# Kernel tuning notes

Measured on AMD Instinct MI355X. Metric: run time of the kernel, lower is better.

The kernel has to match this reference:

```python
import jax, jax.numpy as jnp
import numpy as np

CURVE = 1.0
TAU = 0.5
NB_RF = 64


def _mnorm(x):
    # Minkowski (Lorentz) inner product of x with itself, keepdims: [..., 1]
    return -x[..., :1] ** 2 + jnp.sum(x[..., 1:] ** 2, axis=-1, keepdims=True)


def _hyp_linear(x, W, b, c=CURVE):
    # HypLinear: linear map on space part, time recomputed to stay on hyperboloid.
    # x: [N, Din], W: [H, Din, Ds], b: [H, Ds] -> [H, N, Ds+1]
    space = jnp.einsum('nd,hds->hns', x, W) + b[:, None, :]
    time = jnp.sqrt(1.0 / c + jnp.sum(space ** 2, axis=-1, keepdims=True))
    return jnp.concatenate([time, space], axis=-1)


def _softmax_kernel(data, proj, tau=TAU, c=CURVE, eps=1e-8):
    # FAVOR+ style positive random-feature transform with hyperbolic time correction.
    t = data[..., :1]          # [H, N, 1] Lorentz time component
    s = data[..., 1:]          # [H, N, D-1] space components
    m = 1.0 / jnp.sqrt(jnp.float32(proj.shape[0]))
    wx = jnp.exp(jnp.einsum('hnd,dm->hnm', s, proj) / jnp.sqrt(jnp.float32(tau)))
    front = jnp.exp(((1.0 / c) / tau - t ** 2 / tau) / 2.0) * m + eps
    return wx * front          # [H, N, NB_RF]


def _kernelized(q, k, v, proj, c=CURVE):
    # O(N) linear attention: sum_n k'(n) v(n) then q' @ summary, plus Lorentz renorm.
    qp = _softmax_kernel(q, proj)
    kp = _softmax_kernel(k, proj)
    last = jnp.einsum('hnm,hnd->hmd', kp, v)      # [H, NB_RF, D]
    z = jnp.einsum('hnm,hmd->hnd', qp, last)      # [H, Nq, D]
    coeff = (1.0 / jnp.sqrt(c)) / jnp.sqrt(jnp.abs(_mnorm(z) + 1e-7))
    return z * coeff


def _mobius_add(a, b, c=CURVE):
    ab = jnp.sum(a * b, axis=-1, keepdims=True)
    a2 = jnp.sum(a * a, axis=-1, keepdims=True)
    b2 = jnp.sum(b * b, axis=-1, keepdims=True)
    num = (1.0 + 2.0 * c * ab + c * b2) * a + (1.0 - c * a2) * b
    den = 1.0 + 2.0 * c * ab + c * c * a2 * b2
    return num / (den + 1e-7)


def _hyper_agg(t, c=CURVE):
    # hyperbolic_mean with uniform 1/H weights: Lorentz centroid over heads.
    m = jnp.mean(t, axis=0)                       # [N, D]
    return jnp.sqrt(1.0 / c) * m / jnp.sqrt(jnp.abs(_mnorm(m)) + 1e-7)


def setup_inputs() -> dict:
    H, Din, Ds = 4, 257, 256
    Nu, Ni = 20000, 20000
    # Structured projection matrix: vstacked transposed orthogonal 64x64 blocks,
    # rows rescaled by chi-distributed norms (scaling=0 in the torch code).
    rng = np.random.default_rng(0)
    blocks = []
    for _ in range(Ds // NB_RF):
        q, _ = np.linalg.qr(rng.standard_normal((NB_RF, NB_RF)))
        blocks.append(q.T)
    final = np.vstack(blocks)                     # [Ds, NB_RF]
    mult = np.linalg.norm(rng.standard_normal((Ds, NB_RF)), axis=1)
    proj = jnp.asarray((mult[:, None] * final).astype(np.float32))
    key = jax.random.key(0)
    ks = jax.random.split(key, 5)
    u = jax.random.normal(ks[0], (Nu, Din), dtype=jnp.float32) * 0.3
    i = jax.random.normal(ks[1], (Ni, Din), dtype=jnp.float32) * 0.3
    Wk = jax.random.normal(ks[2], (H, Din, Ds), dtype=jnp.float32) * 0.01
    Wq = jax.random.normal(ks[3], (H, Din, Ds), dtype=jnp.float32) * 0.01
    Wv = jax.random.normal(ks[4], (H, Din, Ds), dtype=jnp.float32) * 0.01
    bk = jnp.zeros((H, Ds), dtype=jnp.float32)
    bq = jnp.zeros((H, Ds), dtype=jnp.float32)
    bv = jnp.zeros((H, Ds), dtype=jnp.float32)
    return {"u": u, "i": i, "Wk": Wk, "bk": bk, "Wq": Wq, "bq": bq,
            "Wv": Wv, "bv": bv, "proj": proj}


def reference(u, i, Wk, bk, Wq, bq, Wv, bv, proj):
    u_key = _hyp_linear(u, Wk, bk)
    i_key = _hyp_linear(i, Wk, bk)
    u_query = _hyp_linear(u, Wq, bq)
    i_query = _hyp_linear(i, Wq, bq)
    u_value = _hyp_linear(u, Wv, bv)
    i_value = _hyp_linear(i, Wv, bv)
    _u_value = _kernelized(u_query, i_key, i_value, proj)
    _i_value = _kernelized(i_query, u_key, u_value, proj)
    u_out = _mobius_add(u_value, _u_value)
    i_out = _mobius_add(i_value, _i_value)
    return _hyper_agg(u_out), _hyper_agg(i_out)
```

## Files before the change

kernel.cpp:

```cpp
#include <hip/hip_runtime.h>
#include <hip/hip_bf16.h>

#define HH 4
#define NR 20000
#define DIN 257
#define DS 256
#define MF 64
#define KP 288
#define VP 264
#define LTP 272
#define ZST 276
#define LKC 25

typedef __bf16 bf16;
typedef bf16 bf16x8 __attribute__((ext_vector_type(8)));
typedef bf16 bf16x4 __attribute__((ext_vector_type(4)));
typedef bf16 bf16x2 __attribute__((ext_vector_type(2)));
typedef float f32x4 __attribute__((ext_vector_type(4)));
typedef unsigned int u32x4 __attribute__((ext_vector_type(4)));

__global__ void cvt_x_kernel(const float* __restrict__ xA, const float* __restrict__ xB,
                             bf16* __restrict__ xbA, bf16* __restrict__ xbB) {
  const int n = blockIdx.x, k = threadIdx.x;
  const float* x = blockIdx.y ? xB : xA;
  bf16* xb = blockIdx.y ? xbB : xbA;
  bf16 v = (bf16)0.f;
  if (k < DIN) v = (bf16)x[(long)n * DIN + k];
  else if (k == DIN) v = (bf16)1.f;
  xb[(long)n * KP + k] = v;
}

__global__ void cvt_w_kernel(const float* __restrict__ Wq, const float* __restrict__ Wk,
                             const float* __restrict__ Wv, bf16* __restrict__ WbTq,
                             bf16* __restrict__ WbTk, bf16* __restrict__ WbTv) {
  const int which = blockIdx.y;
  const int h = blockIdx.x >> 8, n = blockIdx.x & 255, k = threadIdx.x;
  const float* W = which == 0 ? Wq : (which == 1 ? Wk : Wv);
  bf16* o = which == 0 ? WbTq : (which == 1 ? WbTk : WbTv);
  o[((long)h * 256 + n) * KP + k] =
      (k < DIN) ? (bf16)W[((long)h * DIN + k) * DS + n] : (bf16)0.f;
}

__global__ void cvt_wp_kernel(const float* __restrict__ Wq, const float* __restrict__ Wk,
                              const float* __restrict__ bq, const float* __restrict__ bk,
                              const float* __restrict__ proj, bf16* __restrict__ WpT) {
  const int k = blockIdx.x, h = blockIdx.y, which = blockIdx.z, m = threadIdx.x;
  const float* W = which ? Wk : Wq;
  const float* bb = which ? bk : bq;
  float acc = 0.f;
  if (k < DIN) {
    const float* wr = W + ((long)h * DIN + k) * DS;
#pragma unroll 8
    for (int d = 0; d < DS; d++) acc = fmaf(wr[d], proj[(long)d * MF + m], acc);
  } else if (k == DIN) {
    const float* br = bb + (long)h * DS;
#pragma unroll 8
    for (int d = 0; d < DS; d++) acc = fmaf(br[d], proj[(long)d * MF + m], acc);
  }
  WpT[(((long)which * HH + h) * MF + m) * KP + k] = (bf16)acc;
}

__device__ __forceinline__ void gl_lds16(const bf16* g, bf16* l) {
  __builtin_amdgcn_global_load_lds(
      (const __attribute__((address_space(1))) unsigned int*)g,
      (__attribute__((address_space(3))) unsigned int*)l, 16, 0, 0);
}

__global__ __launch_bounds__(256) void proj4_kernel(
    const bf16* __restrict__ xbA, const bf16* __restrict__ xbB,
    const bf16* __restrict__ WbTq, const bf16* __restrict__ WbTk,
    const bf16* __restrict__ WbTv,
    const float* __restrict__ bq, const float* __restrict__ bk,
    const float* __restrict__ bv,
    bf16* __restrict__ voA, bf16* __restrict__ voB, float* __restrict__ fr)
{
  __shared__ __align__(16) char smem[40960];
  bf16* Ab = (bf16*)smem;
  bf16* Bb = (bf16*)(smem + 8192);
  float (*rs)[4] = (float(*)[4])smem;

  const int t = threadIdx.x;
  const int zh = blockIdx.x;
  const int h = zh & 3;
  const int z = zh >> 2;
  const int n0 = blockIdx.y * 64;
  const bf16* xb = (z == 1 || z >= 4) ? xbB : xbA;
  const bf16* WbT = (z < 2) ? WbTv : ((z == 2 || z == 4) ? WbTq : WbTk);
  const float* bsel = (z < 2) ? bv : ((z == 2 || z == 4) ? bq : bk);
  const int w = t >> 6, lane = t & 63;
  const int m16 = lane & 15, q = lane >> 4;
  const bf16* wbh = WbT + (long)h * 256 * KP;

  const int rsub = w * 16 + (lane >> 2);
  const int cb = (lane & 3) * 8;
  const bf16* gA = xb + (long)min(n0 + rsub, NR - 1) * KP + cb;
  const bf16* gB = wbh + (long)rsub * KP + cb;

#define STAGE(buf, c)                                                        \
  do {                                                                       \
    const int _k0 = (c) * 32;                                                \
    gl_lds16(gA + _k0, Ab + (buf) * 2048 + w * 512);                         \
    _Pragma("unroll")                                                        \
    for (int e = 0; e < 4; e++)                                              \
      gl_lds16(gB + (long)e * 64 * KP + _k0,                                 \
               Bb + (buf) * 8192 + e * 2048 + w * 512);                      \
  } while (0)

  f32x4 acc[4][4] = {};
  STAGE(0, 0);

  for (int c = 0; c < 9; c++) {
    const int cur = c & 1;
    __syncthreads();
    if (c < 8) STAGE(1 - cur, c + 1);

    bf16x8 af[4], bfj[4];
#pragma unroll
    for (int i = 0; i < 4; i++)
      af[i] = *(const bf16x8*)(Ab + cur * 2048 + (i * 16 + m16) * 32 + q * 8);
#pragma unroll
    for (int j = 0; j < 4; j++)
      bfj[j] = *(const bf16x8*)(Bb + cur * 8192 + (w * 64 + j * 16 + m16) * 32 + q * 8);
#pragma unroll
    for (int i = 0; i < 4; i++)
#pragma unroll
      for (int j = 0; j < 4; j++)
        acc[i][j] = __builtin_amdgcn_mfma_f32_16x16x32_bf16(af[i], bfj[j], acc[i][j], 0, 0, 0);
  }
#undef STAGE

  __syncthreads();

  float bias[4];
#pragma unroll
  for (int j = 0; j < 4; j++) bias[j] = bsel[h * DS + w * 64 + j * 16 + m16];
#pragma unroll
  for (int i = 0; i < 4; i++)
#pragma unroll
    for (int r = 0; r < 4; r++) {
      float s = 0.f;
#pragma unroll
      for (int j = 0; j < 4; j++) {
        acc[i][j][r] += bias[j];
        s = fmaf(acc[i][j][r], acc[i][j][r], s);
      }
      for (int off = 1; off < 16; off <<= 1) s += __shfl_xor(s, off);
      if (m16 == 0) rs[i * 16 + q * 4 + r][w] = s;
    }
  __syncthreads();

  if (z < 2) {
    bf16* vout = z ? voB : voA;
    if (t < 64) {
      const float ss = rs[t][0] + rs[t][1] + rs[t][2] + rs[t][3];
      if (n0 + t < NR) vout[((long)h * NR + n0 + t) * VP] = (bf16)sqrtf(1.f + ss);
    }
#pragma unroll
    for (int i = 0; i < 4; i++) {
      const int row = i * 16 + q * 4;
#pragma unroll
      for (int r = 0; r < 4; r++) {
        const int rg = n0 + row + r;
        if (rg < NR) {
          bf16* vo = vout + ((long)h * NR + rg) * VP + 1 + w * 64 + m16;
          vo[0] = (bf16)acc[i][0][r]; vo[16] = (bf16)acc[i][1][r];
          vo[32] = (bf16)acc[i][2][r]; vo[48] = (bf16)acc[i][3][r];
        }
      }
    }
  } else {
    if (t < 64 && n0 + t < NR) {
      const float ss = rs[t][0] + rs[t][1] + rs[t][2] + rs[t][3];
      fr[((long)(z - 2) * HH + h) * NR + n0 + t] = 0.125f * __expf(-ss) + 1e-8f;
    }
  }
}

__global__ __launch_bounds__(256) void feat_kernel(
    const bf16* __restrict__ xbA, const bf16* __restrict__ xbB,
    const bf16* __restrict__ WpT, const float* __restrict__ fr,
    bf16* __restrict__ qpA, bf16* __restrict__ kpA,
    bf16* __restrict__ qpB, bf16* __restrict__ kpB)
{
  const int t = threadIdx.x;
  const int ch = blockIdx.x;
  const int h = ch & 3;
  const int c = ch >> 2;
  const int n0 = blockIdx.y * 128;
  const bf16* xb = (c >= 2) ? xbB : xbA;
  const bf16* wp = WpT + (((long)(c & 1) * HH + h) * MF) * KP;
  bf16* fout = (c == 0) ? qpA : (c == 1) ? kpA : (c == 2) ? qpB : kpB;
  const float* frc = fr + ((long)c * HH + h) * NR;
  const int w = t >> 6, lane = t & 63;
  const int m16 = lane & 15, q = lane >> 4;
  const int r0 = w * 32;

  const bf16* aptr[2];
#pragma unroll
  for (int i = 0; i < 2; i++)
    aptr[i] = xb + (long)min(n0 + r0 + i * 16 + m16, NR - 1) * KP + q * 8;
  const bf16* bptr[4];
#pragma unroll
  for (int j = 0; j < 4; j++)
    bptr[j] = wp + (long)(j * 16 + m16) * KP + q * 8;

  f32x4 acc[2][4] = {};
  bf16x8 afc[2], bfc[4], afn[2], bfn[4];
#pragma unroll
  for (int i = 0; i < 2; i++) afc[i] = *(const bf16x8*)(aptr[i]);
#pragma unroll
  for (int j = 0; j < 4; j++) bfc[j] = *(const bf16x8*)(bptr[j]);

  for (int c9 = 0; c9 < 9; c9++) {
    if (c9 < 8) {
      const int k1 = (c9 + 1) * 32;
#pragma unroll
      for (int i = 0; i < 2; i++) afn[i] = *(const bf16x8*)(aptr[i] + k1);
#pragma unroll
      for (int j = 0; j < 4; j++) bfn[j] = *(const bf16x8*)(bptr[j] + k1);
    }
#pragma unroll
    for (int i = 0; i < 2; i++)
#pragma unroll
      for (int j = 0; j < 4; j++)
        acc[i][j] = __builtin_amdgcn_mfma_f32_16x16x32_bf16(afc[i], bfc[j], acc[i][j], 0, 0, 0);
#pragma unroll
    for (int i = 0; i < 2; i++) afc[i] = afn[i];
#pragma unroll
    for (int j = 0; j < 4; j++) bfc[j] = bfn[j];
  }
  const float SQ2 = 1.41421356237309515f;
#pragma unroll
  for (int i = 0; i < 2; i++)
#pragma unroll
    for (int r = 0; r < 4; r++) {
      const int rg = n0 + r0 + i * 16 + q * 4 + r;
      if (rg < NR) {
        const float frv = frc[rg];
        bf16* fo = fout + ((long)h * NR + rg) * MF + m16;
#pragma unroll
        for (int j = 0; j < 4; j++)
          fo[j * 16] = (bf16)(__expf(SQ2 * acc[i][j][r]) * frv);
      }
    }
}

__global__ __launch_bounds__(256) void last3_kernel(
    const bf16* __restrict__ vA, const bf16* __restrict__ fA,
    const bf16* __restrict__ vB, const bf16* __restrict__ fB,
    float* __restrict__ part)
{
  __shared__ unsigned int Va[64 * 17];
  __shared__ unsigned int Fa[64 * 17];
  const int t = threadIdx.x;
  const int dt = blockIdx.x, kc = blockIdx.y, z = blockIdx.z;
  const int side = z >> 2, h = z & 3;
  const bf16* v = side ? vB : vA;
  const bf16* f = side ? fB : fA;
  const int d0 = dt * 64;
  const int w = t >> 6, lane = t & 63;
  const int m16 = lane & 15, q = lane >> 4;
  const int np = t >> 4, xg = (t & 15) * 4;
  f32x4 acc[4] = {};

  for (int c = 0; c < LKC; c++) {
    const int n0 = (kc * LKC + c) * 32;
    {
      const bf16* s0 = v + ((long)h * NR + n0 + 2 * np) * VP + d0 + xg;
      const bf16* s1 = s0 + VP;
      if (d0 + xg + 3 < DIN) {
        const bf16x4 a0 = *(const bf16x4*)s0;
        const bf16x4 a1 = *(const bf16x4*)s1;
#pragma unroll
        for (int e = 0; e < 4; e++) {
          bf16x2 p; p[0] = a0[e]; p[1] = a1[e];
          Va[(xg + e) * 17 + np] = __builtin_bit_cast(unsigned int, p);
        }
      } else {
#pragma unroll
        for (int e = 0; e < 4; e++) {
          bf16 a0 = (bf16)0.f, a1 = (bf16)0.f;
          if (d0 + xg + e < DIN) { a0 = s0[e]; a1 = s1[e]; }
          bf16x2 p; p[0] = a0; p[1] = a1;
          Va[(xg + e) * 17 + np] = __builtin_bit_cast(unsigned int, p);
        }
      }
    }
    {
      const bf16* s0 = f + ((long)h * NR + n0 + 2 * np) * MF + xg;
      const bf16x4 f0 = *(const bf16x4*)s0;
      const bf16x4 f1 = *(const bf16x4*)(s0 + MF);
#pragma unroll
      for (int e = 0; e < 4; e++) {
        bf16x2 p; p[0] = f0[e]; p[1] = f1[e];
        Fa[(xg + e) * 17 + np] = __builtin_bit_cast(unsigned int, p);
      }
    }
    __syncthreads();
    u32x4 bw;
#pragma unroll
    for (int c4 = 0; c4 < 4; c4++) bw[c4] = Fa[(w * 16 + m16) * 17 + q * 4 + c4];
    const bf16x8 bv = __builtin_bit_cast(bf16x8, bw);
#pragma unroll
    for (int i = 0; i < 4; i++) {
      u32x4 aw;
#pragma unroll
      for (int c4 = 0; c4 < 4; c4++) aw[c4] = Va[(i * 16 + m16) * 17 + q * 4 + c4];
      acc[i] = __builtin_amdgcn_mfma_f32_16x16x32_bf16(
          __builtin_bit_cast(bf16x8, aw), bv, acc[i], 0, 0, 0);
    }
    __syncthreads();
  }
  float* pp = part + ((long)(z * LKC + kc) * 5 + dt) * 4096;
#pragma unroll
  for (int i = 0; i < 4; i++)
#pragma unroll
    for (int r = 0; r < 4; r++)
      pp[(i * 16 + q * 4 + r) * 64 + w * 16 + m16] = acc[i][r];
}

__global__ void reduce_last4(const float* __restrict__ part,
                             bf16* __restrict__ hiU, bf16* __restrict__ loU,
                             bf16* __restrict__ hiI, bf16* __restrict__ loI) {
  const int d = blockIdx.x, zz = blockIdx.y, m = threadIdx.x;
  const int side = zz >> 2, h = zz & 3;
  const int dt = d >> 6, dl = d & 63;
  float s = 0.f;
#pragma unroll 5
  for (int kc = 0; kc < LKC; kc++)
    s += part[((long)(zz * LKC + kc) * 5 + dt) * 4096 + dl * 64 + m];
  bf16* hi = side ? hiI : hiU;
  bf16* lo = side ? loI : loU;
  const bf16 hv = (bf16)s;
  hi[((long)h * LTP + d) * MF + m] = hv;
  lo[((long)h * LTP + d) * MF + m] = (bf16)(s - (float)hv);
}

__global__ __launch_bounds__(256) void fuse3_kernel(
    const bf16* __restrict__ qpA, const bf16* __restrict__ vA,
    const bf16* __restrict__ hiA, const bf16* __restrict__ loA,
    const bf16* __restrict__ qpB, const bf16* __restrict__ vB,
    const bf16* __restrict__ hiB, const bf16* __restrict__ loB,
    float* __restrict__ out)
{
  __shared__ __align__(16) float zs[32 * ZST];

  const int side = blockIdx.y;
  const bf16* qp = side ? qpB : qpA;
  const bf16* v = side ? vB : vA;
  const bf16* hi = side ? hiB : hiA;
  const bf16* lo = side ? loB : loA;
  float* o = out + (long)side * NR * DIN;

  const int t = threadIdx.x;
  const int n0 = blockIdx.x * 32;
  const int w = t >> 6, lane = t & 63;
  const int m16 = lane & 15, q = lane >> 4;
  const int erow = t >> 3, ecol = (t & 7) * 4;
  const bool lead = ((t & 7) == 0);
  const int ntile = (w == 0) ? 5 : 4;

  f32x4 macc[8] = {};
  float macc256 = 0.f;

  for (int h = 0; h < HH; h++) {
    const bf16* vr = v + ((long)h * NR + n0 + erow) * VP;
    f32x4 vreg[8];
#pragma unroll
    for (int it = 0; it < 8; it++) {
      const bf16x4 vb = *(const bf16x4*)(vr + it * 32 + ecol);
#pragma unroll
      for (int c = 0; c < 4; c++) vreg[it][c] = (float)vb[c];
    }
    float v256 = lead ? (float)vr[256] : 0.f;

    bf16x8 af[2][2];
#pragma unroll
    for (int i = 0; i < 2; i++)
#pragma unroll
      for (int hf = 0; hf < 2; hf++)
        af[i][hf] = *(const bf16x8*)(qp + ((long)h * NR + n0 + i * 16 + m16) * MF + hf * 32 + q * 8);

    for (int jt = 0; jt < ntile; jt++) {
      const int dt = (jt < 4) ? (w + jt * 4) : 16;
      const int d = dt * 16 + m16;
      const bf16* ph = hi + ((long)h * LTP + d) * MF + q * 8;
      const bf16* pl = lo + ((long)h * LTP + d) * MF + q * 8;
      const bf16x8 bh0 = *(const bf16x8*)ph, bh1 = *(const bf16x8*)(ph + 32);
      const bf16x8 bl0 = *(const bf16x8*)pl, bl1 = *(const bf16x8*)(pl + 32);
#pragma unroll
      for (int i = 0; i < 2; i++) {
        f32x4 a = {0.f, 0.f, 0.f, 0.f};
        a = __builtin_amdgcn_mfma_f32_16x16x32_bf16(af[i][1], bl1, a, 0, 0, 0);
        a = __builtin_amdgcn_mfma_f32_16x16x32_bf16(af[i][0], bl0, a, 0, 0, 0);
        a = __builtin_amdgcn_mfma_f32_16x16x32_bf16(af[i][1], bh1, a, 0, 0, 0);
        a = __builtin_amdgcn_mfma_f32_16x16x32_bf16(af[i][0], bh0, a, 0, 0, 0);
#pragma unroll
        for (int r = 0; r < 4; r++)
          zs[(i * 16 + q * 4 + r) * ZST + d] = a[r];
      }
    }
    __syncthreads();

    f32x4 zreg[8];
    float sz2 = 0.f, svz = 0.f, z0p = 0.f, v02p = 0.f;
#pragma unroll
    for (int it = 0; it < 8; it++) {
      zreg[it] = *(const f32x4*)&zs[erow * ZST + it * 32 + ecol];
#pragma unroll
      for (int c = 0; c < 4; c++) {
        sz2 = fmaf(zreg[it][c], zreg[it][c], sz2);
        svz = fmaf(vreg[it][c], zreg[it][c], svz);
      }
    }
    float z256 = 0.f;
    if (lead) {
      z256 = zs[erow * ZST + 256];
      sz2 = fmaf(z256, z256, sz2);
      svz = fmaf(v256, z256, svz);
      z0p = zreg[0][0];
      v02p = vreg[0][0] * vreg[0][0];
    }
#pragma unroll
    for (int off = 1; off < 8; off <<= 1) {
      sz2 += __shfl_xor(sz2, off);
      svz += __shfl_xor(svz, off);
      z0p += __shfl_xor(z0p, off);
      v02p += __shfl_xor(v02p, off);
    }
    const float a2 = 2.f * v02p - 1.f;
    const float mn = sz2 - 2.f * z0p * z0p;
    const float cf = 1.f / sqrtf(fabsf(mn + 1e-7f));
    const float ab = cf * svz;
    const float b2 = cf * cf * sz2;
    const float den = 1.f + 2.f * ab + a2 * b2;
    const float inv = 0.25f / (den + 1e-7f);
    const float sx = (1.f + 2.f * ab + b2) * inv;
    const float sy = (1.f - a2) * cf * inv;
#pragma unroll
    for (int it = 0; it < 8; it++)
#pragma unroll
      for (int c = 0; c < 4; c++)
        macc[it][c] = fmaf(sx, vreg[it][c], fmaf(sy, zreg[it][c], macc[it][c]));
    if (lead) macc256 = fmaf(sx, v256, fmaf(sy, z256, macc256));
    __syncthreads();
  }

  float sm2 = 0.f, m02p = 0.f;
#pragma unroll
  for (int it = 0; it < 8; it++)
#pragma unroll
    for (int c = 0; c < 4; c++) sm2 = fmaf(macc[it][c], macc[it][c], sm2);
  if (lead) {
    sm2 = fmaf(macc256, macc256, sm2);
    m02p = macc[0][0] * macc[0][0];
  }
#pragma unroll
  for (int off = 1; off < 8; off <<= 1) {
    sm2 += __shfl_xor(sm2, off);
    m02p += __shfl_xor(m02p, off);
  }
  const float fv = 1.f / sqrtf(fabsf(sm2 - 2.f * m02p) + 1e-7f);
  float* orow = o + (long)(n0 + erow) * DIN;
#pragma unroll
  for (int it = 0; it < 8; it++)
#pragma unroll
    for (int c = 0; c < 4; c++) orow[it * 32 + ecol + c] = macc[it][c] * fv;
  if (lead) orow[256] = macc256 * fv;
}

extern "C" void kernel_launch(void* const* d_in, const int* in_sizes, int n_in,
                              void* d_out, int out_size, void* d_ws, size_t ws_size,
                              hipStream_t stream) {
  const float* u    = (const float*)d_in[0];
  const float* ii   = (const float*)d_in[1];
  const float* Wk   = (const float*)d_in[2];
  const float* bk   = (const float*)d_in[3];
  const float* Wq   = (const float*)d_in[4];
  const float* bq   = (const float*)d_in[5];
  const float* Wv   = (const float*)d_in[6];
  const float* bv   = (const float*)d_in[7];
  const float* proj = (const float*)d_in[8];
  float* out = (float*)d_out;

  const long NVB = (long)HH * NR * VP;
  const long NF = (long)HH * NR * MF;
  const long NLT = (long)HH * LTP * MF;
  bf16* v_u = (bf16*)d_ws;
  bf16* v_i = v_u + NVB;
  bf16* qp_u = v_i + NVB;
  bf16* kp_u = qp_u + NF;
  bf16* qp_i = kp_u + NF;
  bf16* kp_i = qp_i + NF;
  bf16* ltHi_u = kp_i + NF;
  bf16* ltLo_u = ltHi_u + NLT;
  bf16* ltHi_i = ltLo_u + NLT;
  bf16* ltLo_i = ltHi_i + NLT;
  bf16* xb_u  = ltLo_i + NLT;
  bf16* xb_i  = xb_u + (long)NR * KP;
  bf16* WbTq  = xb_i + (long)NR * KP;
  bf16* WbTk  = WbTq + 4 * 256 * KP;
  bf16* WbTv  = WbTk + 4 * 256 * KP;
  bf16* WpT   = WbTv + 4 * 256 * KP;
  float* fr   = (float*)(WpT + 8 * 64 * KP);
  float* part = (float*)xb_u;

  cvt_x_kernel<<<dim3(NR, 2), KP, 0, stream>>>(u, ii, xb_u, xb_i);
  cvt_w_kernel<<<dim3(1024, 3), KP, 0, stream>>>(Wq, Wk, Wv, WbTq, WbTk, WbTv);
  cvt_wp_kernel<<<dim3(KP, HH, 2), 64, 0, stream>>>(Wq, Wk, bq, bk, proj, WpT);

  proj4_kernel<<<dim3(24, (NR + 63) / 64), 256, 0, stream>>>(
      xb_u, xb_i, WbTq, WbTk, WbTv, bq, bk, bv, v_u, v_i, fr);
  feat_kernel<<<dim3(16, (NR + 127) / 128), 256, 0, stream>>>(
      xb_u, xb_i, WpT, fr, qp_u, kp_u, qp_i, kp_i);

  last3_kernel<<<dim3(5, LKC, 8), 256, 0, stream>>>(v_i, kp_i, v_u, kp_u, part);
  reduce_last4<<<dim3(LTP, 8), 64, 0, stream>>>(part, ltHi_u, ltLo_u, ltHi_i, ltLo_i);

  fuse3_kernel<<<dim3(NR / 32, 2), 256, 0, stream>>>(
      qp_u, v_u, ltHi_u, ltLo_u, qp_i, v_i, ltHi_i, ltLo_i, out);
}
```

Before: 459.9 us.

## Fuse random-feature projection into the projection GEMM kernel, drop feat_kernel

The q/k projection blocks of proj4_kernel now also run a 64-column MFMA against the precomputed W·proj matrix, reusing the already-staged A fragments. They compute the time-correction factor into shared memory and write the exp features directly. This removes the separate feat_kernel launch, its re-read of the bf16 inputs, and the fr round-trip through global memory. In exchange, the q/k blocks do extra MFMAs and uncached global loads of WpT inside the main loop, and take an extra barrier. This adds imbalance against the value blocks.

Result: faster. 439.1 us (-4.5%).

```diff
diff --git a/kernel.cpp b/kernel.cpp
--- a/kernel.cpp
+++ b/kernel.cpp
@@ -69,15 +69,18 @@
 __global__ __launch_bounds__(256) void proj4_kernel(
     const bf16* __restrict__ xbA, const bf16* __restrict__ xbB,
     const bf16* __restrict__ WbTq, const bf16* __restrict__ WbTk,
-    const bf16* __restrict__ WbTv,
+    const bf16* __restrict__ WbTv, const bf16* __restrict__ WpT,
     const float* __restrict__ bq, const float* __restrict__ bk,
     const float* __restrict__ bv,
-    bf16* __restrict__ voA, bf16* __restrict__ voB, float* __restrict__ fr)
+    bf16* __restrict__ voA, bf16* __restrict__ voB,
+    bf16* __restrict__ qpA, bf16* __restrict__ kpA,
+    bf16* __restrict__ qpB, bf16* __restrict__ kpB)
 {
   __shared__ __align__(16) char smem[40960];
   bf16* Ab = (bf16*)smem;
   bf16* Bb = (bf16*)(smem + 8192);
   float (*rs)[4] = (float(*)[4])smem;
+  float* frl = (float*)(smem + 2048);
 
   const int t = threadIdx.x;
   const int zh = blockIdx.x;
@@ -96,6 +99,9 @@
   const bf16* gA = xb + (long)min(n0 + rsub, NR - 1) * KP + cb;
   const bf16* gB = wbh + (long)rsub * KP + cb;
 
+  const int which = (z == 2 || z == 4) ? 0 : 1;
+  const bf16* gWp = WpT + (((long)which * HH + h) * MF + (w * 16 + m16)) * KP + q * 8;
+
 #define STAGE(buf, c)                                                        \
   do {                                                                       \
     const int _k0 = (c) * 32;                                                \
@@ -107,6 +113,7 @@
   } while (0)
 
   f32x4 acc[4][4] = {};
+  f32x4 acc5[4] = {};
   STAGE(0, 0);
 
   for (int c = 0; c < 9; c++) {
@@ -126,6 +133,12 @@
 #pragma unroll
       for (int j = 0; j < 4; j++)
         acc[i][j] = __builtin_amdgcn_mfma_f32_16x16x32_bf16(af[i], bfj[j], acc[i][j], 0, 0, 0);
+    if (z >= 2) {
+      const bf16x8 bf5 = *(const bf16x8*)(gWp + c * 32);
+#pragma unroll
+      for (int i = 0; i < 4; i++)
+        acc5[i] = __builtin_amdgcn_mfma_f32_16x16x32_bf16(af[i], bf5, acc5[i], 0, 0, 0);
+    }
   }
 #undef STAGE
 
@@ -169,80 +182,27 @@
       }
     }
   } else {
-    if (t < 64 && n0 + t < NR) {
+    if (t < 64) {
       const float ss = rs[t][0] + rs[t][1] + rs[t][2] + rs[t][3];
-      fr[((long)(z - 2) * HH + h) * NR + n0 + t] = 0.125f * __expf(-ss) + 1e-8f;
-    }
-  }
-}
-
-__global__ __launch_bounds__(256) void feat_kernel(
-    const bf16* __restrict__ xbA, const bf16* __restrict__ xbB,
-    const bf16* __restrict__ WpT, const float* __restrict__ fr,
-    bf16* __restrict__ qpA, bf16* __restrict__ kpA,
-    bf16* __restrict__ qpB, bf16* __restrict__ kpB)
-{
-  const int t = threadIdx.x;
-  const int ch = blockIdx.x;
-  const int h = ch & 3;
-  const int c = ch >> 2;
-  const int n0 = blockIdx.y * 128;
-  const bf16* xb = (c >= 2) ? xbB : xbA;
-  const bf16* wp = WpT + (((long)(c & 1) * HH + h) * MF) * KP;
-  bf16* fout = (c == 0) ? qpA : (c == 1) ? kpA : (c == 2) ? qpB : kpB;
-  const float* frc = fr + ((long)c * HH + h) * NR;
-  const int w = t >> 6, lane = t & 63;
-  const int m16 = lane & 15, q = lane >> 4;
-  const int r0 = w * 32;
-
-  const bf16* aptr[2];
-#pragma unroll
-  for (int i = 0; i < 2; i++)
-    aptr[i] = xb + (long)min(n0 + r0 + i * 16 + m16, NR - 1) * KP + q * 8;
-  const bf16* bptr[4];
-#pragma unroll
-  for (int j = 0; j < 4; j++)
-    bptr[j] = wp + (long)(j * 16 + m16) * KP + q * 8;
-
-  f32x4 acc[2][4] = {};
-  bf16x8 afc[2], bfc[4], afn[2], bfn[4];
-#pragma unroll
-  for (int i = 0; i < 2; i++) afc[i] = *(const bf16x8*)(aptr[i]);
-#pragma unroll
-  for (int j = 0; j < 4; j++) bfc[j] = *(const bf16x8*)(bptr[j]);
-
-  for (int c9 = 0; c9 < 9; c9++) {
-    if (c9 < 8) {
-      const int k1 = (c9 + 1) * 32;
-#pragma unroll
-      for (int i = 0; i < 2; i++) afn[i] = *(const bf16x8*)(aptr[i] + k1);
-#pragma unroll
-      for (int j = 0; j < 4; j++) bfn[j] = *(const bf16x8*)(bptr[j] + k1);
-    }
-#pragma unroll
-    for (int i = 0; i < 2; i++)
-#pragma unroll
-      for (int j = 0; j < 4; j++)
-        acc[i][j] = __builtin_amdgcn_mfma_f32_16x16x32_bf16(afc[i], bfc[j], acc[i][j], 0, 0, 0);
-#pragma unroll
-    for (int i = 0; i < 2; i++) afc[i] = afn[i];
-#pragma unroll
-    for (int j = 0; j < 4; j++) bfc[j] = bfn[j];
-  }
-  const float SQ2 = 1.41421356237309515f;
-#pragma unroll
-  for (int i = 0; i < 2; i++)
-#pragma unroll
-    for (int r = 0; r < 4; r++) {
-      const int rg = n0 + r0 + i * 16 + q * 4 + r;
-      if (rg < NR) {
-        const float frv = frc[rg];
-        bf16* fo = fout + ((long)h * NR + rg) * MF + m16;
-#pragma unroll
-        for (int j = 0; j < 4; j++)
-          fo[j * 16] = (bf16)(__expf(SQ2 * acc[i][j][r]) * frv);
-      }
-    }
+      frl[t] = 0.125f * __expf(-ss) + 1e-8f;
+    }
+    __syncthreads();
+    bf16* fout = (z == 2) ? qpA : (z == 3) ? kpA : (z == 4) ? qpB : kpB;
+    const float SQ2 = 1.41421356237309515f;
+#pragma unroll
+    for (int i = 0; i < 4; i++) {
+      const int row = i * 16 + q * 4;
+#pragma unroll
+      for (int r = 0; r < 4; r++) {
+        const int rg = n0 + row + r;
+        if (rg < NR) {
+          const float frv = frl[row + r];
+          fout[((long)h * NR + rg) * MF + w * 16 + m16] =
+              (bf16)(__expf(SQ2 * acc5[i][r]) * frv);
+        }
+      }
+    }
+  }
 }
 
 __global__ __launch_bounds__(256) void last3_kernel(
@@ -502,7 +462,6 @@
   bf16* WbTk  = WbTq + 4 * 256 * KP;
   bf16* WbTv  = WbTk + 4 * 256 * KP;
   bf16* WpT   = WbTv + 4 * 256 * KP;
-  float* fr   = (float*)(WpT + 8 * 64 * KP);
   float* part = (float*)xb_u;
 
   cvt_x_kernel<<<dim3(NR, 2), KP, 0, stream>>>(u, ii, xb_u, xb_i);
@@ -510,9 +469,8 @@
   cvt_wp_kernel<<<dim3(KP, HH, 2), 64, 0, stream>>>(Wq, Wk, bq, bk, proj, WpT);
 
   proj4_kernel<<<dim3(24, (NR + 63) / 64), 256, 0, stream>>>(
-      xb_u, xb_i, WbTq, WbTk, WbTv, bq, bk, bv, v_u, v_i, fr);
-  feat_kernel<<<dim3(16, (NR + 127) / 128), 256, 0, stream>>>(
-      xb_u, xb_i, WpT, fr, qp_u, kp_u, qp_i, kp_i);
+      xb_u, xb_i, WbTq, WbTk, WbTv, WpT, bq, bk, bv,
+      v_u, v_i, qp_u, kp_u, qp_i, kp_i);
 
   last3_kernel<<<dim3(5, LKC, 8), 256, 0, stream>>>(v_i, kp_i, v_u, kp_u, part);
   reduce_last4<<<dim3(LTP, 8), 64, 0, stream>>>(part, ltHi_u, ltLo_u, ltHi_i, ltLo_i);
```
